# Optimization experiments

Hardware: AMD Instinct MI355X
Metric: run time of the kernel (lower is better)

Reference implementation:

```python
import jax, jax.numpy as jnp
import numpy as np

D_MODEL = 1024
N_HEADS = 16
HEAD_DIM = D_MODEL // N_HEADS


def setup_inputs() -> dict:
    key = jax.random.key(0)
    ks = jax.random.split(key, 9)
    B, S = 2, 2048
    s = 1.0 / np.sqrt(D_MODEL)
    x = jax.random.normal(ks[0], (B, S, D_MODEL), dtype=jnp.float32)
    Wq = jax.random.normal(ks[1], (N_HEADS, D_MODEL, HEAD_DIM), dtype=jnp.float32) * s
    Wk = jax.random.normal(ks[2], (N_HEADS, D_MODEL, HEAD_DIM), dtype=jnp.float32) * s
    Wv = jax.random.normal(ks[3], (N_HEADS, D_MODEL, HEAD_DIM), dtype=jnp.float32) * s
    bq = jax.random.normal(ks[4], (N_HEADS, HEAD_DIM), dtype=jnp.float32) * s
    bk = jax.random.normal(ks[5], (N_HEADS, HEAD_DIM), dtype=jnp.float32) * s
    bv = jax.random.normal(ks[6], (N_HEADS, HEAD_DIM), dtype=jnp.float32) * s
    Wp = jax.random.normal(ks[7], (D_MODEL, D_MODEL), dtype=jnp.float32) * s
    bp = jax.random.normal(ks[8], (D_MODEL,), dtype=jnp.float32) * s
    return {"x": x, "Wq": Wq, "Wk": Wk, "Wv": Wv, "bq": bq, "bk": bk, "bv": bv, "Wp": Wp, "bp": bp}


def reference(x, Wq, Wk, Wv, bq, bk, bv, Wp, bp):
    # Per-head projections batched over heads: [B,S,D] x [H,D,E] -> [B,H,S,E]
    Q = jnp.einsum('bsd,hde->bhse', x, Wq) + bq[None, :, None, :]
    K = jnp.einsum('bsd,hde->bhse', x, Wk) + bk[None, :, None, :]
    V = jnp.einsum('bsd,hde->bhse', x, Wv) + bv[None, :, None, :]
    scores = jnp.einsum('bhse,bhte->bhst', Q, K) / jnp.sqrt(jnp.asarray(HEAD_DIM, x.dtype))
    attn = jax.nn.softmax(scores, axis=-1)          # [B,H,S,S]
    out = jnp.einsum('bhst,bhte->bhse', attn, V)    # [B,H,S,E]
    B, H, S, E = out.shape
    concat = out.transpose(0, 2, 1, 3).reshape(B, S, H * E)  # concat heads along feature
    return concat @ Wp.T + bp
```

## Files before the change

kernel.cpp:

```cpp
#include <hip/hip_runtime.h>
#include <hip/hip_bf16.h>

typedef __attribute__((ext_vector_type(8))) short short8;
typedef __attribute__((ext_vector_type(4))) short svec4;
typedef __attribute__((ext_vector_type(4))) float float4_t;
typedef __attribute__((ext_vector_type(8))) _Float16 half8;

#define D_MODEL 1024
#define N_HEADS 16
#define HEAD_DIM 64
#define B_SZ 2
#define SEQ 2048
#define M_ROWS (B_SZ*SEQ)
#define NQKV 3072
#define SC_LOG2E 0.18033688011112042f

__device__ __forceinline__ unsigned short f2bf(float f) {
  unsigned u = __float_as_uint(f);
  u += 0x7FFFu + ((u >> 16) & 1u);
  return (unsigned short)(u >> 16);
}

__device__ __forceinline__ unsigned short f2h(float f) {
  _Float16 h = (_Float16)f;
  return *(unsigned short*)&h;
}

__device__ __forceinline__ void gl_lds16(const unsigned short* g, unsigned short* l) {
  __builtin_amdgcn_global_load_lds(
      (const __attribute__((address_space(1))) unsigned int*)(size_t)g,
      (__attribute__((address_space(3))) unsigned int*)(unsigned int)(size_t)l,
      16, 0, 0);
}

__global__ void prep(const float* __restrict__ x, const float* __restrict__ Wp,
                     const float* __restrict__ Wq, const float* __restrict__ Wk,
                     const float* __restrict__ Wv,
                     unsigned short* __restrict__ xb, unsigned short* __restrict__ Wpb,
                     unsigned short* __restrict__ Wall) {
  __shared__ float t[16][17];
  int bid = blockIdx.x;
  if (bid < 5120) {
    const float* src; unsigned short* dst; int base;
    if (bid < 4096) { src = x;  dst = xb;  base = bid * 1024 + threadIdx.x * 4; }
    else            { src = Wp; dst = Wpb; base = (bid - 4096) * 1024 + threadIdx.x * 4; }
    float4 v = *(const float4*)(src + base);
    dst[base + 0] = f2bf(v.x);
    dst[base + 1] = f2bf(v.y);
    dst[base + 2] = f2bf(v.z);
    dst[base + 3] = f2bf(v.w);
  } else {
    int u = bid - 5120;
    int sel = u >> 12;
    u &= 4095;
    const float* W = sel == 0 ? Wq : (sel == 1 ? Wk : Wv);
    int d0 = (u & 63) * 16, e0 = ((u >> 6) & 3) * 16, hh = u >> 8;
    int tx = threadIdx.x & 15, ty = threadIdx.x >> 4;
    t[ty][tx] = W[hh * (D_MODEL * HEAD_DIM) + (d0 + ty) * HEAD_DIM + e0 + tx];
    __syncthreads();
    Wall[(size_t)(sel * 1024 + hh * 64 + e0 + ty) * D_MODEL + d0 + tx] = f2bf(t[tx][ty]);
  }
}

__global__ __launch_bounds__(256) void qkv_gemm(const unsigned short* __restrict__ xb,
                                                const unsigned short* __restrict__ Wall,
                                                const float* __restrict__ bq,
                                                const float* __restrict__ bk,
                                                const float* __restrict__ bv,
                                                unsigned short* __restrict__ Qb,
                                                unsigned short* __restrict__ Kb,
                                                unsigned short* __restrict__ Vtb) {
  __shared__ unsigned short As[128 * 32], Bs[128 * 32];
  __shared__ __align__(16) unsigned short Stage[4][16 * 72];
  const int m0 = blockIdx.x * 128, n0 = blockIdx.y * 128;
  const int lane = threadIdx.x & 63, w = threadIdx.x >> 6;
  const int l16 = lane & 15, quad = lane >> 4;
  const int wm = w & 1, wn = w >> 1;
  const int ldrow = lane >> 2, ldcol = (lane & 3) * 8;
  const unsigned short* ga0 = xb + (size_t)(m0 + w * 32 + ldrow) * D_MODEL + ldcol;
  const unsigned short* ga1 = ga0 + 16 * D_MODEL;
  const unsigned short* gb0 = Wall + (size_t)(n0 + w * 32 + ldrow) * D_MODEL + ldcol;
  const unsigned short* gb1 = gb0 + 16 * D_MODEL;
  unsigned short* lA0 = As + (w * 2 + 0) * 512;
  unsigned short* lA1 = As + (w * 2 + 1) * 512;
  unsigned short* lB0 = Bs + (w * 2 + 0) * 512;
  unsigned short* lB1 = Bs + (w * 2 + 1) * 512;
  float4_t acc[4][4];
  float4_t z = {0.f, 0.f, 0.f, 0.f};
#pragma unroll
  for (int i = 0; i < 4; i++)
#pragma unroll
    for (int j = 0; j < 4; j++) acc[i][j] = z;
  for (int k0 = 0; k0 < D_MODEL; k0 += 32) {
    __syncthreads();
    gl_lds16(ga0 + k0, lA0);
    gl_lds16(ga1 + k0, lA1);
    gl_lds16(gb0 + k0, lB0);
    gl_lds16(gb1 + k0, lB1);
    __syncthreads();
    short8 af[4], bf[4];
#pragma unroll
    for (int i = 0; i < 4; i++) af[i] = *(const short8*)&As[(wm * 64 + i * 16 + l16) * 32 + quad * 8];
#pragma unroll
    for (int j = 0; j < 4; j++) bf[j] = *(const short8*)&Bs[(wn * 64 + j * 16 + l16) * 32 + quad * 8];
#pragma unroll
    for (int i = 0; i < 4; i++)
#pragma unroll
      for (int j = 0; j < 4; j++)
        acc[i][j] = __builtin_amdgcn_mfma_f32_16x16x32_bf16(af[i], bf[j], acc[i][j], 0, 0, 0);
  }
  const int nb = n0 + wn * 64;
  const int sel = nb >> 10;
  const int h = (nb >> 6) & 15;
  const float* bias = sel == 0 ? bq : (sel == 1 ? bk : bv);
  const int mbase = m0 + wm * 64;
  const int bb = mbase >> 11;
  const size_t bh = (size_t)(bb * N_HEADS + h);
  if (sel == 2) {
    unsigned short* vs = &Stage[w][0];
    const size_t vbase = bh * (32 * 4096) + (size_t)((mbase >> 6) & 31) * 4096;
    const int e8 = lane >> 3, ch = lane & 7;
#pragma unroll
    for (int j = 0; j < 4; j++) {
      float be = bias[h * 64 + j * 16 + l16];
#pragma unroll
      for (int i = 0; i < 4; i++)
#pragma unroll
        for (int r = 0; r < 4; r++)
          vs[l16 * 72 + i * 16 + quad * 4 + r] = f2h(acc[i][j][r] + be);
#pragma unroll
      for (int rd = 0; rd < 2; rd++) {
        int er = rd * 8 + e8;
        short8 val = *(const short8*)(vs + er * 72 + ch * 8);
        *(short8*)(Vtb + vbase + (size_t)(j * 16 + er) * 64 + ch * 8) = val;
      }
    }
  } else {
    unsigned short* st = &Stage[w][0];
    unsigned short* dst = (sel == 0) ? Qb : Kb;
    const float qsc = (sel == 0) ? SC_LOG2E : 1.0f;
    const size_t rowbase = bh * SEQ + (mbase & (SEQ - 1));
    const int r2 = lane >> 1, c2 = lane & 1;
#pragma unroll
    for (int j = 0; j < 4; j++) {
      float be = bias[h * 64 + j * 16 + l16];
#pragma unroll
      for (int i = 0; i < 4; i++)
#pragma unroll
        for (int r = 0; r < 4; r++)
          st[(i * 16 + quad * 4 + r) * 18 + l16] = f2bf((acc[i][j][r] + be) * qsc);
#pragma unroll
      for (int p = 0; p < 2; p++) {
        int row = p * 32 + r2;
        short8 val = *(const short8*)(st + row * 18 + c2 * 8);
        *(short8*)(dst + (rowbase + row) * HEAD_DIM + j * 16 + c2 * 8) = val;
      }
    }
  }
}

__global__ __launch_bounds__(256) void attn_kernel(const unsigned short* __restrict__ Q,
                                                   const unsigned short* __restrict__ K,
                                                   const unsigned short* __restrict__ Vt,
                                                   unsigned short* __restrict__ concat) {
  __shared__ __align__(16) unsigned short Ks0[64 * 72], Ks1[64 * 72];
  __shared__ __align__(16) unsigned short Vs0[64 * 72], Vs1[64 * 72];
  const int b = blockIdx.z, h = blockIdx.y;
  const int tid = threadIdx.x;
  const int lane = tid & 63, w = tid >> 6;
  const int l16 = lane & 15, quad = lane >> 4;
  const size_t bh = (size_t)(b * N_HEADS + h);
  const int q0 = blockIdx.x * 128 + w * 32;
  float4_t z = {0.f, 0.f, 0.f, 0.f};

  short8 aq[2][2];
#pragma unroll
  for (int rg = 0; rg < 2; rg++)
#pragma unroll
    for (int hf = 0; hf < 2; hf++)
      aq[rg][hf] = *(const short8*)(Q + (bh * SEQ + q0 + rg * 16 + l16) * HEAD_DIM + hf * 32 + quad * 8);

  const int krow = tid >> 2, kch = (tid & 3) * 8;
  const unsigned short* kg = K + (bh * SEQ + krow) * HEAD_DIM + kch;
  const int ktw = krow * 72 + kch;
  const int vt0 = (tid & 3) * 16, vt1 = vt0 + 8;
  const unsigned short* vg = Vt + bh * (32 * 4096) + krow * 64 + vt0;
  const int tp0 = ((vt0 >> 5) << 5) + (((vt0 >> 2) & 3) << 3) + (((vt0 >> 4) & 1) << 2);
  const int tp1 = ((vt1 >> 5) << 5) + (((vt1 >> 2) & 3) << 3) + (((vt1 >> 4) & 1) << 2);
  const int vtw0 = krow * 72 + tp0, vtw1 = krow * 72 + tp1;

  float4_t o[2][4];
#pragma unroll
  for (int rg = 0; rg < 2; rg++)
#pragma unroll
    for (int ne = 0; ne < 4; ne++) o[rg][ne] = z;
  float lsp[2] = {0.f, 0.f};

  short8 kreg0 = *(const short8*)kg;
  short8 kreg1 = *(const short8*)(kg + 32);
  short8 vreg0 = *(const short8*)vg;
  short8 vreg1 = *(const short8*)(vg + 8);
  kg += 4096; vg += 4096;

  auto step = [&](unsigned short* kb, unsigned short* vb, int itv) {
    *(short8*)(kb + ktw) = kreg0;
    *(short8*)(kb + ktw + 32) = kreg1;
    svec4 a0 = {vreg0[0], vreg0[1], vreg0[2], vreg0[3]};
    svec4 a1 = {vreg0[4], vreg0[5], vreg0[6], vreg0[7]};
    svec4 b0 = {vreg1[0], vreg1[1], vreg1[2], vreg1[3]};
    svec4 b1 = {vreg1[4], vreg1[5], vreg1[6], vreg1[7]};
    *(svec4*)(vb + vtw0) = a0;
    *(svec4*)(vb + vtw0 + 8) = a1;
    *(svec4*)(vb + vtw1) = b0;
    *(svec4*)(vb + vtw1 + 8) = b1;
    __syncthreads();
    if (itv < 31) {
      kreg0 = *(const short8*)kg;
      kreg1 = *(const short8*)(kg + 32);
      vreg0 = *(const short8*)vg;
      vreg1 = *(const short8*)(vg + 8);
      kg += 4096; vg += 4096;
    }
#pragma unroll
    for (int p = 0; p < 2; p++) {
      float4_t s[2][2];
#pragma unroll
      for (int tcl = 0; tcl < 2; tcl++) {
        int tc = 2 * p + tcl;
        short8 kf0 = *(const short8*)(kb + (tc * 16 + l16) * 72 + quad * 8);
        short8 kf1 = *(const short8*)(kb + (tc * 16 + l16) * 72 + 32 + quad * 8);
#pragma unroll
        for (int rg = 0; rg < 2; rg++) {
          s[tcl][rg] = __builtin_amdgcn_mfma_f32_16x16x32_bf16(kf0, aq[rg][0], z, 0, 0, 0);
          s[tcl][rg] = __builtin_amdgcn_mfma_f32_16x16x32_bf16(kf1, aq[rg][1], s[tcl][rg], 0, 0, 0);
        }
      }
      half8 vf[4];
#pragma unroll
      for (int ne = 0; ne < 4; ne++)
        vf[ne] = *(const half8*)(vb + (ne * 16 + l16) * 72 + p * 32 + quad * 8);
#pragma unroll
      for (int rg = 0; rg < 2; rg++) {
        float pv[8];
#pragma unroll
        for (int r = 0; r < 4; r++) {
          pv[r]     = __builtin_amdgcn_exp2f(s[0][rg][r]);
          pv[4 + r] = __builtin_amdgcn_exp2f(s[1][rg][r]);
        }
        lsp[rg] += ((pv[0] + pv[1]) + (pv[2] + pv[3])) + ((pv[4] + pv[5]) + (pv[6] + pv[7]));
        half8 pa = {(_Float16)pv[0], (_Float16)pv[1], (_Float16)pv[2], (_Float16)pv[3],
                    (_Float16)pv[4], (_Float16)pv[5], (_Float16)pv[6], (_Float16)pv[7]};
#pragma unroll
        for (int ne = 0; ne < 4; ne++)
          o[rg][ne] = __builtin_amdgcn_mfma_f32_16x16x32_f16(pa, vf[ne], o[rg][ne], 0, 0, 0);
      }
    }
  };

  for (int it2 = 0; it2 < 16; ++it2) {
    step(Ks0, Vs0, 2 * it2);
    step(Ks1, Vs1, 2 * it2 + 1);
  }

  float lsf[2];
#pragma unroll
  for (int rg = 0; rg < 2; rg++) {
    float v = lsp[rg];
    v += __shfl_xor(v, 16, 64);
    v += __shfl_xor(v, 32, 64);
    lsf[rg] = v;
  }
#pragma unroll
  for (int rg = 0; rg < 2; rg++) {
#pragma unroll
    for (int r = 0; r < 4; r++) {
      float li = 1.0f / __shfl(lsf[rg], quad * 4 + r, 64);
      int sr = q0 + rg * 16 + quad * 4 + r;
#pragma unroll
      for (int ne = 0; ne < 4; ne++)
        concat[((size_t)(b * SEQ + sr)) * D_MODEL + h * 64 + ne * 16 + l16] = f2bf(o[rg][ne][r] * li);
    }
  }
}

__global__ __launch_bounds__(256) void out_gemm(const unsigned short* __restrict__ cb,
                                                const unsigned short* __restrict__ Wpb,
                                                const float* __restrict__ bp,
                                                float* __restrict__ out) {
  __shared__ unsigned short As[128 * 32], Bs[64 * 32];
  const int m0 = blockIdx.x * 128, n0 = blockIdx.y * 64;
  const int lane = threadIdx.x & 63, w = threadIdx.x >> 6;
  const int l16 = lane & 15, quad = lane >> 4;
  const int ldrow = lane >> 2, ldcol = (lane & 3) * 8;
  const unsigned short* ga0 = cb + (size_t)(m0 + w * 32 + ldrow) * D_MODEL + ldcol;
  const unsigned short* ga1 = ga0 + 16 * D_MODEL;
  const unsigned short* gb0 = Wpb + (size_t)(n0 + w * 16 + ldrow) * D_MODEL + ldcol;
  unsigned short* lA0 = As + (w * 2 + 0) * 512;
  unsigned short* lA1 = As + (w * 2 + 1) * 512;
  unsigned short* lB0 = Bs + w * 512;
  float4_t acc[2][4];
  float4_t z = {0.f, 0.f, 0.f, 0.f};
#pragma unroll
  for (int i = 0; i < 2; i++)
#pragma unroll
    for (int j = 0; j < 4; j++) acc[i][j] = z;
  for (int k0 = 0; k0 < D_MODEL; k0 += 32) {
    __syncthreads();
    gl_lds16(ga0 + k0, lA0);
    gl_lds16(ga1 + k0, lA1);
    gl_lds16(gb0 + k0, lB0);
    __syncthreads();
    short8 af[2], bf[4];
#pragma unroll
    for (int i = 0; i < 2; i++) af[i] = *(const short8*)&As[(w * 32 + i * 16 + l16) * 32 + quad * 8];
#pragma unroll
    for (int j = 0; j < 4; j++) bf[j] = *(const short8*)&Bs[(j * 16 + l16) * 32 + quad * 8];
#pragma unroll
    for (int i = 0; i < 2; i++)
#pragma unroll
      for (int j = 0; j < 4; j++)
        acc[i][j] = __builtin_amdgcn_mfma_f32_16x16x32_bf16(af[i], bf[j], acc[i][j], 0, 0, 0);
  }
#pragma unroll
  for (int i = 0; i < 2; i++)
#pragma unroll
    for (int j = 0; j < 4; j++)
#pragma unroll
      for (int r = 0; r < 4; r++) {
        int m = m0 + w * 32 + i * 16 + quad * 4 + r;
        int oc = n0 + j * 16 + l16;
        out[(size_t)m * D_MODEL + oc] = acc[i][j][r] + bp[oc];
      }
}

extern "C" void kernel_launch(void* const* d_in, const int* in_sizes, int n_in,
                              void* d_out, int out_size, void* d_ws, size_t ws_size,
                              hipStream_t stream) {
  const float* x  = (const float*)d_in[0];
  const float* Wq = (const float*)d_in[1];
  const float* Wk = (const float*)d_in[2];
  const float* Wv = (const float*)d_in[3];
  const float* bq = (const float*)d_in[4];
  const float* bk = (const float*)d_in[5];
  const float* bv = (const float*)d_in[6];
  const float* Wp = (const float*)d_in[7];
  const float* bp = (const float*)d_in[8];
  float* out = (float*)d_out;

  char* ws = (char*)d_ws;
  size_t off = 0;
  auto alloc = [&](size_t bytes) -> void* {
    void* p = ws + off;
    off += (bytes + 255) & ~(size_t)255;
    return p;
  };
  unsigned short* xb   = (unsigned short*)alloc((size_t)M_ROWS * D_MODEL * 2);
  unsigned short* Wall = (unsigned short*)alloc((size_t)NQKV * D_MODEL * 2);
  unsigned short* Wpb  = (unsigned short*)alloc((size_t)D_MODEL * D_MODEL * 2);
  unsigned short* Qb   = (unsigned short*)alloc((size_t)B_SZ * N_HEADS * SEQ * HEAD_DIM * 2);
  unsigned short* Kb   = (unsigned short*)alloc((size_t)B_SZ * N_HEADS * SEQ * HEAD_DIM * 2);
  unsigned short* Vtb  = (unsigned short*)alloc((size_t)B_SZ * N_HEADS * SEQ * HEAD_DIM * 2);
  unsigned short* cbuf = (unsigned short*)alloc((size_t)B_SZ * SEQ * D_MODEL * 2);

  prep<<<17408, 256, 0, stream>>>(x, Wp, Wq, Wk, Wv, xb, Wpb, Wall);

  qkv_gemm<<<dim3(M_ROWS / 128, NQKV / 128), 256, 0, stream>>>(xb, Wall, bq, bk, bv, Qb, Kb, Vtb);

  attn_kernel<<<dim3(SEQ / 128, N_HEADS, B_SZ), 256, 0, stream>>>(Qb, Kb, Vtb, cbuf);

  out_gemm<<<dim3(M_ROWS / 128, D_MODEL / 64), 256, 0, stream>>>(cbuf, Wpb, bp, out);
}
```

Baseline: 189.0 us.

## Load K fragments directly from global, remap blocks per XCD, pack P with cvt_pkrtz

The attention kernel drops the K shared-memory staging and has each wave load its K MFMA fragments straight from global memory, which removes the LDS writes and reads for K. The grid becomes 1D, and blocks are remapped so that each XCD works on a contiguous set of (batch, head) pairs, which should improve L2 reuse of K/V. It also adds s_setprio around the MFMA bursts and uses packed round-toward-zero f16 conversion for P. In exchange, each wave now issues redundant global K loads, and round-toward-zero slightly changes numerics.

```diff
diff --git a/kernel.cpp b/kernel.cpp
--- a/kernel.cpp
+++ b/kernel.cpp
@@ -163,14 +163,16 @@
                                                    const unsigned short* __restrict__ K,
                                                    const unsigned short* __restrict__ Vt,
                                                    unsigned short* __restrict__ concat) {
-  __shared__ __align__(16) unsigned short Ks0[64 * 72], Ks1[64 * 72];
   __shared__ __align__(16) unsigned short Vs0[64 * 72], Vs1[64 * 72];
-  const int b = blockIdx.z, h = blockIdx.y;
+  const int lin = blockIdx.x;
+  const int xcd = lin & 7, slot = lin >> 3;
+  const int bh = xcd * 4 + (slot >> 4);
+  const int b = bh >> 4, h = bh & 15;
+  const int qt = slot & 15;
   const int tid = threadIdx.x;
   const int lane = tid & 63, w = tid >> 6;
   const int l16 = lane & 15, quad = lane >> 4;
-  const size_t bh = (size_t)(b * N_HEADS + h);
-  const int q0 = blockIdx.x * 128 + w * 32;
+  const int q0 = qt * 128 + w * 32;
   float4_t z = {0.f, 0.f, 0.f, 0.f};
 
   short8 aq[2][2];
@@ -178,16 +180,16 @@
   for (int rg = 0; rg < 2; rg++)
 #pragma unroll
     for (int hf = 0; hf < 2; hf++)
-      aq[rg][hf] = *(const short8*)(Q + (bh * SEQ + q0 + rg * 16 + l16) * HEAD_DIM + hf * 32 + quad * 8);
-
-  const int krow = tid >> 2, kch = (tid & 3) * 8;
-  const unsigned short* kg = K + (bh * SEQ + krow) * HEAD_DIM + kch;
-  const int ktw = krow * 72 + kch;
+      aq[rg][hf] = *(const short8*)(Q + ((size_t)bh * SEQ + q0 + rg * 16 + l16) * HEAD_DIM + hf * 32 + quad * 8);
+
+  const unsigned short* kgp = K + ((size_t)bh * SEQ + l16) * HEAD_DIM + quad * 8;
+
+  const int vrow = tid >> 2;
   const int vt0 = (tid & 3) * 16, vt1 = vt0 + 8;
-  const unsigned short* vg = Vt + bh * (32 * 4096) + krow * 64 + vt0;
+  const unsigned short* vg = Vt + (size_t)bh * (32 * 4096) + vrow * 64 + vt0;
   const int tp0 = ((vt0 >> 5) << 5) + (((vt0 >> 2) & 3) << 3) + (((vt0 >> 4) & 1) << 2);
   const int tp1 = ((vt1 >> 5) << 5) + (((vt1 >> 2) & 3) << 3) + (((vt1 >> 4) & 1) << 2);
-  const int vtw0 = krow * 72 + tp0, vtw1 = krow * 72 + tp1;
+  const int vtw0 = vrow * 72 + tp0, vtw1 = vrow * 72 + tp1;
 
   float4_t o[2][4];
 #pragma unroll
@@ -196,15 +198,11 @@
     for (int ne = 0; ne < 4; ne++) o[rg][ne] = z;
   float lsp[2] = {0.f, 0.f};
 
-  short8 kreg0 = *(const short8*)kg;
-  short8 kreg1 = *(const short8*)(kg + 32);
   short8 vreg0 = *(const short8*)vg;
   short8 vreg1 = *(const short8*)(vg + 8);
-  kg += 4096; vg += 4096;
-
-  auto step = [&](unsigned short* kb, unsigned short* vb, int itv) {
-    *(short8*)(kb + ktw) = kreg0;
-    *(short8*)(kb + ktw + 32) = kreg1;
+  vg += 4096;
+
+  auto step = [&](unsigned short* vb, int itv) {
     svec4 a0 = {vreg0[0], vreg0[1], vreg0[2], vreg0[3]};
     svec4 a1 = {vreg0[4], vreg0[5], vreg0[6], vreg0[7]};
     svec4 b0 = {vreg1[0], vreg1[1], vreg1[2], vreg1[3]};
@@ -213,28 +211,33 @@
     *(svec4*)(vb + vtw0 + 8) = a1;
     *(svec4*)(vb + vtw1) = b0;
     *(svec4*)(vb + vtw1 + 8) = b1;
+    short8 kf[4][2];
+#pragma unroll
+    for (int tc = 0; tc < 4; tc++) {
+      kf[tc][0] = *(const short8*)(kgp + tc * 16 * HEAD_DIM);
+      kf[tc][1] = *(const short8*)(kgp + tc * 16 * HEAD_DIM + 32);
+    }
+    kgp += 64 * HEAD_DIM;
     __syncthreads();
     if (itv < 31) {
-      kreg0 = *(const short8*)kg;
-      kreg1 = *(const short8*)(kg + 32);
       vreg0 = *(const short8*)vg;
       vreg1 = *(const short8*)(vg + 8);
-      kg += 4096; vg += 4096;
+      vg += 4096;
     }
 #pragma unroll
     for (int p = 0; p < 2; p++) {
       float4_t s[2][2];
+      __builtin_amdgcn_s_setprio(1);
 #pragma unroll
       for (int tcl = 0; tcl < 2; tcl++) {
         int tc = 2 * p + tcl;
-        short8 kf0 = *(const short8*)(kb + (tc * 16 + l16) * 72 + quad * 8);
-        short8 kf1 = *(const short8*)(kb + (tc * 16 + l16) * 72 + 32 + quad * 8);
 #pragma unroll
         for (int rg = 0; rg < 2; rg++) {
-          s[tcl][rg] = __builtin_amdgcn_mfma_f32_16x16x32_bf16(kf0, aq[rg][0], z, 0, 0, 0);
-          s[tcl][rg] = __builtin_amdgcn_mfma_f32_16x16x32_bf16(kf1, aq[rg][1], s[tcl][rg], 0, 0, 0);
+          s[tcl][rg] = __builtin_amdgcn_mfma_f32_16x16x32_bf16(kf[tc][0], aq[rg][0], z, 0, 0, 0);
+          s[tcl][rg] = __builtin_amdgcn_mfma_f32_16x16x32_bf16(kf[tc][1], aq[rg][1], s[tcl][rg], 0, 0, 0);
         }
       }
+      __builtin_amdgcn_s_setprio(0);
       half8 vf[4];
 #pragma unroll
       for (int ne = 0; ne < 4; ne++)
@@ -248,18 +251,24 @@
           pv[4 + r] = __builtin_amdgcn_exp2f(s[1][rg][r]);
         }
         lsp[rg] += ((pv[0] + pv[1]) + (pv[2] + pv[3])) + ((pv[4] + pv[5]) + (pv[6] + pv[7]));
-        half8 pa = {(_Float16)pv[0], (_Float16)pv[1], (_Float16)pv[2], (_Float16)pv[3],
-                    (_Float16)pv[4], (_Float16)pv[5], (_Float16)pv[6], (_Float16)pv[7]};
+        union { unsigned u[4]; half8 hh; } pk;
+        pk.u[0] = __builtin_bit_cast(unsigned, __builtin_amdgcn_cvt_pkrtz(pv[0], pv[1]));
+        pk.u[1] = __builtin_bit_cast(unsigned, __builtin_amdgcn_cvt_pkrtz(pv[2], pv[3]));
+        pk.u[2] = __builtin_bit_cast(unsigned, __builtin_amdgcn_cvt_pkrtz(pv[4], pv[5]));
+        pk.u[3] = __builtin_bit_cast(unsigned, __builtin_amdgcn_cvt_pkrtz(pv[6], pv[7]));
+        half8 pa = pk.hh;
+        __builtin_amdgcn_s_setprio(1);
 #pragma unroll
         for (int ne = 0; ne < 4; ne++)
           o[rg][ne] = __builtin_amdgcn_mfma_f32_16x16x32_f16(pa, vf[ne], o[rg][ne], 0, 0, 0);
+        __builtin_amdgcn_s_setprio(0);
       }
     }
   };
 
   for (int it2 = 0; it2 < 16; ++it2) {
-    step(Ks0, Vs0, 2 * it2);
-    step(Ks1, Vs1, 2 * it2 + 1);
+    step(Vs0, 2 * it2);
+    step(Vs1, 2 * it2 + 1);
   }
 
   float lsf[2];
@@ -366,7 +375,7 @@
 
   qkv_gemm<<<dim3(M_ROWS / 128, NQKV / 128), 256, 0, stream>>>(xb, Wall, bq, bk, bv, Qb, Kb, Vtb);
 
-  attn_kernel<<<dim3(SEQ / 128, N_HEADS, B_SZ), 256, 0, stream>>>(Qb, Kb, Vtb, cbuf);
+  attn_kernel<<<512, 256, 0, stream>>>(Qb, Kb, Vtb, cbuf);
 
   out_gemm<<<dim3(M_ROWS / 128, D_MODEL / 64), 256, 0, stream>>>(cbuf, Wpb, bp, out);
 }
```

Result: slower. 206.8 us (+9.4%).
